# Kernel tuning notes

Hardware: AMD Instinct MI355X
Metric: run time of the kernel (lower is better)

## Reference

```python
import jax, jax.numpy as jnp
import numpy as np

MARGIN = 0.2
EPS = 1e-6  # torch.pairwise_distance default eps added to (x1 - x2)


def setup_inputs() -> dict:
    key = jax.random.key(0)
    k1, k2 = jax.random.split(key)
    N, D = 8192, 128
    x = jax.random.normal(k1, (N, D), dtype=jnp.float32)
    target = jax.random.randint(k2, (N,), 0, 1000)
    return {"x": x, "target": target}


def _pairwise_dist(x):
    # torch.pairwise_distance(x.unsqueeze(0), x.unsqueeze(1)):
    #   diff[i, j] = x[j] - x[i] + EPS ; dist[i, j] = ||diff[i, j]||_2
    # Expanded quadratic form avoids the [N, N, D] diff tensor:
    #   ||a - b + e||^2 = ||a||^2 + ||b||^2 - 2 a.b + 2e*sum(a - b) + D*e^2
    sq = jnp.sum(x * x, axis=1)          # [N]
    s = jnp.sum(x, axis=1)               # [N]
    dot = x @ x.T                        # [N, N]
    D = x.shape[1]
    d2 = (sq[None, :] + sq[:, None] - 2.0 * dot
          + 2.0 * EPS * (s[None, :] - s[:, None]) + D * EPS * EPS)
    return jnp.sqrt(jnp.maximum(d2, 0.0))


def reference(x, target):
    N = x.shape[0]
    dist = _pairwise_dist(x)                                 # [N, N]
    same = target[None, :] == target[:, None]                # [N, N] bool
    pos_mask = (same & ~jnp.eye(N, dtype=bool)).astype(x.dtype)
    hardest_pos = jnp.max(pos_mask * dist, axis=1, keepdims=True)  # [N, 1]
    neg_mask = (~same).astype(x.dtype)
    max_neg = jnp.max(dist, axis=1, keepdims=True)           # [N, 1]
    anchor_neg = dist + max_neg * (1.0 - neg_mask)           # push positives up
    hardest_neg = jnp.min(anchor_neg, axis=1, keepdims=True) # [N, 1]
    loss = jax.nn.relu(hardest_pos - hardest_neg + MARGIN)
    return jnp.mean(loss)
```

## Files before the change

kernel.cpp:

```cpp
#include <hip/hip_runtime.h>

#define N 8192
#define Dk 128
#define EPSC 1e-6f
#define MARGIN 0.2f

#define BI 64
#define BJ 128
#define JSPLIT 4
#define LDA 136

typedef __attribute__((ext_vector_type(8))) short bf16x8;
typedef __attribute__((ext_vector_type(4))) float f32x4;

__device__ __forceinline__ unsigned short f2bf(float f) {
    unsigned u = __float_as_uint(f);
    u = (u + 0x7FFFu + ((u >> 16) & 1u)) >> 16;
    return (unsigned short)u;
}
__device__ __forceinline__ unsigned enc(float f) {
    unsigned u = __float_as_uint(f);
    return (u & 0x80000000u) ? ~u : (u | 0x80000000u);
}
__device__ __forceinline__ float dec(unsigned u) {
    return __uint_as_float((u & 0x80000000u) ? (u & 0x7FFFFFFFu) : ~u);
}

__global__ void prep_kernel(const float* __restrict__ x,
                            unsigned short* __restrict__ Xb,
                            float* __restrict__ P, float* __restrict__ Q,
                            unsigned* __restrict__ wsHp, unsigned* __restrict__ wsMn) {
    int gtid = blockIdx.x * blockDim.x + threadIdx.x;
    int row = gtid >> 6;
    int lane = gtid & 63;
    const float2 v = *reinterpret_cast<const float2*>(&x[row * Dk + lane * 2]);
    float sq = v.x * v.x + v.y * v.y;
    float s = v.x + v.y;
    ushort2 o;
    o.x = f2bf(v.x);
    o.y = f2bf(v.y);
    *reinterpret_cast<ushort2*>(&Xb[row * Dk + lane * 2]) = o;
#pragma unroll
    for (int m = 32; m >= 1; m >>= 1) {
        sq += __shfl_xor(sq, m);
        s += __shfl_xor(s, m);
    }
    if (lane == 0) {
        P[row] = sq - 2.0f * EPSC * s;
        Q[row] = sq + 2.0f * EPSC * s + (float)Dk * EPSC * EPSC;
        wsHp[row] = 0x007FFFFFu;
        wsMn[row] = 0xFF800000u;
    }
}

__global__ __launch_bounds__(256) void main_kernel(
        const unsigned short* __restrict__ Xb,
        const float* __restrict__ Q,
        const int* __restrict__ tgt,
        unsigned* __restrict__ wsHp, unsigned* __restrict__ wsMn) {
    __shared__ unsigned short As[BI * LDA];
    __shared__ unsigned short Bs[BJ * LDA];
    __shared__ float Qs[BJ];
    __shared__ int Ts[BJ];

    const int tid = threadIdx.x;
    const int w = tid >> 6;
    const int lane = tid & 63;
    const int n = lane & 15;
    const int q = lane >> 4;

    const int ig = (int)blockIdx.x >> 2;
    const int js = (int)blockIdx.x & 3;
    const int i0 = ig * BI;
    const int jstart = js * (N / JSPLIT);

    const uint4* Xb4 = reinterpret_cast<const uint4*>(Xb);

#pragma unroll
    for (int it = 0; it < 4; ++it) {
        int idx = tid + 256 * it;
        int r = idx >> 4, c = idx & 15;
        uint4 v = Xb4[(i0 + r) * 16 + c];
        *reinterpret_cast<uint4*>(&As[r * LDA + c * 8]) = v;
    }

    int tslot[16];
#pragma unroll
    for (int ti = 0; ti < 4; ++ti) {
        int4 t4 = *reinterpret_cast<const int4*>(&tgt[i0 + 16 * ti + 4 * q]);
        tslot[ti * 4 + 0] = t4.x;
        tslot[ti * 4 + 1] = t4.y;
        tslot[ti * 4 + 2] = t4.z;
        tslot[ti * 4 + 3] = t4.w;
    }

    float hp[16], mn[16];
#pragma unroll
    for (int s = 0; s < 16; ++s) {
        hp[s] = -INFINITY;
        mn[s] = INFINITY;
    }

    int aoff[4], boff[2];
#pragma unroll
    for (int ti = 0; ti < 4; ++ti) aoff[ti] = (16 * ti + n) * LDA + q * 8;
#pragma unroll
    for (int tj = 0; tj < 2; ++tj) boff[tj] = (32 * w + 16 * tj + n) * LDA + q * 8;

    for (int step = 0; step < (N / JSPLIT) / BJ; ++step) {
        const int jbase = jstart + step * BJ;
        __syncthreads();
#pragma unroll
        for (int it = 0; it < 8; ++it) {
            int idx = tid + 256 * it;
            int r = idx >> 4, c = idx & 15;
            uint4 v = Xb4[(jbase + r) * 16 + c];
            *reinterpret_cast<uint4*>(&Bs[r * LDA + c * 8]) = v;
        }
        if (tid < BJ) Qs[tid] = Q[jbase + tid];
        else Ts[tid - BJ] = tgt[jbase + tid - BJ];
        __syncthreads();

        f32x4 acc[4][2];
#pragma unroll
        for (int ti = 0; ti < 4; ++ti)
#pragma unroll
            for (int tj = 0; tj < 2; ++tj) acc[ti][tj] = 0.0f;

#pragma unroll
        for (int kk = 0; kk < 4; ++kk) {
            bf16x8 b0 = *reinterpret_cast<const bf16x8*>(&Bs[boff[0] + kk * 32]);
            bf16x8 b1 = *reinterpret_cast<const bf16x8*>(&Bs[boff[1] + kk * 32]);
#pragma unroll
            for (int ti = 0; ti < 4; ++ti) {
                bf16x8 a = *reinterpret_cast<const bf16x8*>(&As[aoff[ti] + kk * 32]);
                acc[ti][0] = __builtin_amdgcn_mfma_f32_16x16x32_bf16(a, b0, acc[ti][0], 0, 0, 0);
                acc[ti][1] = __builtin_amdgcn_mfma_f32_16x16x32_bf16(a, b1, acc[ti][1], 0, 0, 0);
            }
        }

#pragma unroll
        for (int tj = 0; tj < 2; ++tj) {
            int col = 32 * w + 16 * tj + n;
            float Qv = Qs[col];
            int tv = Ts[col];
#pragma unroll
            for (int ti = 0; ti < 4; ++ti) {
#pragma unroll
                for (int r = 0; r < 4; ++r) {
                    float val = fmaf(-2.0f, acc[ti][tj][r], Qv);
                    int sidx = ti * 4 + r;
                    bool sm = (tv == tslot[sidx]);
                    hp[sidx] = sm ? fmaxf(hp[sidx], val) : hp[sidx];
                    mn[sidx] = sm ? mn[sidx] : fminf(mn[sidx], val);
                }
            }
        }
    }

#pragma unroll
    for (int m = 1; m <= 8; m <<= 1) {
#pragma unroll
        for (int s = 0; s < 16; ++s) {
            hp[s] = fmaxf(hp[s], __shfl_xor(hp[s], m));
            mn[s] = fminf(mn[s], __shfl_xor(mn[s], m));
        }
    }
    if (n == 0) {
#pragma unroll
        for (int ti = 0; ti < 4; ++ti) {
#pragma unroll
            for (int r = 0; r < 4; ++r) {
                int i = i0 + 16 * ti + 4 * q + r;
                atomicMax(&wsHp[i], enc(hp[ti * 4 + r]));
                atomicMin(&wsMn[i], enc(mn[ti * 4 + r]));
            }
        }
    }
}

__global__ void finish_kernel(const float* __restrict__ P,
                              const unsigned* __restrict__ wsHp,
                              const unsigned* __restrict__ wsMn,
                              float* __restrict__ out) {
    int i = blockIdx.x * 256 + threadIdx.x;
    float Pi = P[i];
    float hp = sqrtf(fmaxf(Pi + dec(wsHp[i]), 0.0f));
    float hn = sqrtf(fmaxf(Pi + dec(wsMn[i]), 0.0f));
    float loss = fmaxf(hp - hn + MARGIN, 0.0f) * (1.0f / (float)N);
#pragma unroll
    for (int m = 32; m >= 1; m >>= 1) loss += __shfl_xor(loss, m);
    __shared__ float wsum[4];
    int lane = threadIdx.x & 63, wv = threadIdx.x >> 6;
    if (lane == 0) wsum[wv] = loss;
    __syncthreads();
    if (threadIdx.x == 0) atomicAdd(out, wsum[0] + wsum[1] + wsum[2] + wsum[3]);
}

extern "C" void kernel_launch(void* const* d_in, const int* in_sizes, int n_in,
                              void* d_out, int out_size, void* d_ws, size_t ws_size,
                              hipStream_t stream) {
    const float* x = (const float*)d_in[0];
    const int* tgt = (const int*)d_in[1];
    float* out = (float*)d_out;

    char* ws = (char*)d_ws;
    const size_t xb_bytes = (size_t)N * Dk * 2;
    unsigned short* Xb = (unsigned short*)ws;
    float* P = (float*)(ws + xb_bytes);
    float* Q = (float*)(ws + xb_bytes + (size_t)N * 4);
    unsigned* wsHp = (unsigned*)(ws + xb_bytes + (size_t)N * 8);
    unsigned* wsMn = (unsigned*)(ws + xb_bytes + (size_t)N * 12);

    hipMemsetAsync(d_out, 0, sizeof(float), stream);
    prep_kernel<<<N / 4, 256, 0, stream>>>(x, Xb, P, Q, wsHp, wsMn);
    main_kernel<<<(N / BI) * JSPLIT, 256, 0, stream>>>(Xb, Q, tgt, wsHp, wsMn);
    finish_kernel<<<N / 256, 256, 0, stream>>>(P, wsHp, wsMn, out);
}
```

Baseline: 103.6 us.

## Rework pairwise-distance kernel with register A tiles, swizzled direct-to-LDS loads, and fused epilogue

The main kernel now uses 128x128 tiles with A fragments held in registers and B tiles loaded straight into LDS through global_load_lds, using an XOR-swizzled layout that the prep kernel writes. The prep kernel also stores a pre-scaled -2x copy, so the accumulator can start at Q and the epilogue needs no FMA, and it packs Q with the target label. The epilogue uses a wave ballot to skip the positive path when no lane shares a label. The finish kernel becomes a single block, which removes the memset and the atomic. The larger register tile raises register pressure, and the extra scaled copy doubles the bf16 workspace.

Result: faster. 98.32 us (-5.1%).

```diff
diff --git a/kernel.cpp b/kernel.cpp
--- a/kernel.cpp
+++ b/kernel.cpp
@@ -5,11 +5,6 @@
 #define EPSC 1e-6f
 #define MARGIN 0.2f
 
-#define BI 64
-#define BJ 128
-#define JSPLIT 4
-#define LDA 136
-
 typedef __attribute__((ext_vector_type(8))) short bf16x8;
 typedef __attribute__((ext_vector_type(4))) float f32x4;
 
@@ -26,72 +21,84 @@
     return __uint_as_float((u & 0x80000000u) ? (u & 0x7FFFFFFFu) : ~u);
 }
 
-__global__ void prep_kernel(const float* __restrict__ x,
-                            unsigned short* __restrict__ Xb,
-                            float* __restrict__ P, float* __restrict__ Q,
+__device__ __forceinline__ void gl_lds16(const void* src, void* lds_dst) {
+    __builtin_amdgcn_global_load_lds(
+        (const __attribute__((address_space(1))) unsigned*)src,
+        (__attribute__((address_space(3))) unsigned*)lds_dst, 16, 0, 0);
+}
+
+__global__ void prep_kernel(const float* __restrict__ x, const int* __restrict__ tgt,
+                            unsigned short* __restrict__ XbA, unsigned short* __restrict__ XbB,
+                            uint2* __restrict__ QT, float* __restrict__ P,
                             unsigned* __restrict__ wsHp, unsigned* __restrict__ wsMn) {
-    int gtid = blockIdx.x * blockDim.x + threadIdx.x;
-    int row = gtid >> 6;
-    int lane = gtid & 63;
-    const float2 v = *reinterpret_cast<const float2*>(&x[row * Dk + lane * 2]);
-    float sq = v.x * v.x + v.y * v.y;
+    int row = blockIdx.x * 4 + (threadIdx.x >> 6);
+    int l = threadIdx.x & 63;
+    const float2 v = *reinterpret_cast<const float2*>(&x[row * Dk + l * 2]);
+    float sq = fmaf(v.x, v.x, v.y * v.y);
     float s = v.x + v.y;
-    ushort2 o;
-    o.x = f2bf(v.x);
-    o.y = f2bf(v.y);
-    *reinterpret_cast<ushort2*>(&Xb[row * Dk + lane * 2]) = o;
+    ushort2 a, b;
+    a.x = f2bf(v.x);
+    a.y = f2bf(v.y);
+    b.x = f2bf(-2.0f * v.x);
+    b.y = f2bf(-2.0f * v.y);
+    int c_phys = (l >> 2) ^ (row & 7);
+    int off = row * Dk + c_phys * 8 + 2 * (l & 3);
+    *reinterpret_cast<ushort2*>(&XbA[off]) = a;
+    *reinterpret_cast<ushort2*>(&XbB[off]) = b;
 #pragma unroll
     for (int m = 32; m >= 1; m >>= 1) {
         sq += __shfl_xor(sq, m);
         s += __shfl_xor(s, m);
     }
-    if (lane == 0) {
+    if (l == 0) {
         P[row] = sq - 2.0f * EPSC * s;
-        Q[row] = sq + 2.0f * EPSC * s + (float)Dk * EPSC * EPSC;
+        uint2 qt;
+        qt.x = __float_as_uint(sq + 2.0f * EPSC * s + (float)Dk * EPSC * EPSC);
+        qt.y = (unsigned)tgt[row];
+        QT[row] = qt;
         wsHp[row] = 0x007FFFFFu;
         wsMn[row] = 0xFF800000u;
     }
 }
 
-__global__ __launch_bounds__(256) void main_kernel(
-        const unsigned short* __restrict__ Xb,
-        const float* __restrict__ Q,
-        const int* __restrict__ tgt,
+__global__ __launch_bounds__(256, 2) void main_kernel(
+        const unsigned short* __restrict__ XbA, const unsigned short* __restrict__ XbB,
+        const uint2* __restrict__ QT, const int* __restrict__ tgt,
         unsigned* __restrict__ wsHp, unsigned* __restrict__ wsMn) {
-    __shared__ unsigned short As[BI * LDA];
-    __shared__ unsigned short Bs[BJ * LDA];
-    __shared__ float Qs[BJ];
-    __shared__ int Ts[BJ];
+    __shared__ unsigned short Bs[128 * Dk];
+    __shared__ uint2 QTs[128];
 
     const int tid = threadIdx.x;
     const int w = tid >> 6;
     const int lane = tid & 63;
     const int n = lane & 15;
     const int q = lane >> 4;
-
-    const int ig = (int)blockIdx.x >> 2;
-    const int js = (int)blockIdx.x & 3;
-    const int i0 = ig * BI;
-    const int jstart = js * (N / JSPLIT);
-
-    const uint4* Xb4 = reinterpret_cast<const uint4*>(Xb);
-
-#pragma unroll
-    for (int it = 0; it < 4; ++it) {
-        int idx = tid + 256 * it;
-        int r = idx >> 4, c = idx & 15;
-        uint4 v = Xb4[(i0 + r) * 16 + c];
-        *reinterpret_cast<uint4*>(&As[r * LDA + c * 8]) = v;
-    }
-
-    int tslot[16];
+    const int wi = w >> 1;
+    const int wj = w & 1;
+    const int sw = n & 7;
+
+    const int ig = (int)blockIdx.x >> 3;
+    const int js = (int)blockIdx.x & 7;
+    const int i0 = ig * 128;
+    const int rbase = i0 + 64 * wi;
+
+    bf16x8 Af[4][4];
 #pragma unroll
     for (int ti = 0; ti < 4; ++ti) {
-        int4 t4 = *reinterpret_cast<const int4*>(&tgt[i0 + 16 * ti + 4 * q]);
-        tslot[ti * 4 + 0] = t4.x;
-        tslot[ti * 4 + 1] = t4.y;
-        tslot[ti * 4 + 2] = t4.z;
-        tslot[ti * 4 + 3] = t4.w;
+        const unsigned short* rp = &XbA[(rbase + 16 * ti + n) * Dk];
+#pragma unroll
+        for (int kk = 0; kk < 4; ++kk)
+            Af[ti][kk] = *reinterpret_cast<const bf16x8*>(&rp[((q + 4 * kk) ^ sw) << 3]);
+    }
+
+    int tsl[16];
+#pragma unroll
+    for (int ti = 0; ti < 4; ++ti) {
+        int4 t4 = *reinterpret_cast<const int4*>(&tgt[rbase + 16 * ti + 4 * q]);
+        tsl[4 * ti + 0] = t4.x;
+        tsl[4 * ti + 1] = t4.y;
+        tsl[4 * ti + 2] = t4.z;
+        tsl[4 * ti + 3] = t4.w;
     }
 
     float hp[16], mn[16];
@@ -101,58 +108,75 @@
         mn[s] = INFINITY;
     }
 
-    int aoff[4], boff[2];
-#pragma unroll
-    for (int ti = 0; ti < 4; ++ti) aoff[ti] = (16 * ti + n) * LDA + q * 8;
-#pragma unroll
-    for (int tj = 0; tj < 2; ++tj) boff[tj] = (32 * w + 16 * tj + n) * LDA + q * 8;
-
-    for (int step = 0; step < (N / JSPLIT) / BJ; ++step) {
-        const int jbase = jstart + step * BJ;
+    for (int step = 0; step < 8; ++step) {
+        const int jbase = js * 1024 + step * 128;
         __syncthreads();
 #pragma unroll
-        for (int it = 0; it < 8; ++it) {
-            int idx = tid + 256 * it;
-            int r = idx >> 4, c = idx & 15;
-            uint4 v = Xb4[(jbase + r) * 16 + c];
-            *reinterpret_cast<uint4*>(&Bs[r * LDA + c * 8]) = v;
-        }
-        if (tid < BJ) Qs[tid] = Q[jbase + tid];
-        else Ts[tid - BJ] = tgt[jbase + tid - BJ];
+        for (int t = 0; t < 8; ++t) {
+            const unsigned short* src = &XbB[(jbase + 32 * w + 4 * t) * Dk] + lane * 8;
+            unsigned short* dst = &Bs[(32 * w + 4 * t) * Dk];
+            gl_lds16(src, dst);
+        }
+        if (w == 0) {
+            const unsigned short* src = reinterpret_cast<const unsigned short*>(&QT[jbase]) + lane * 8;
+            gl_lds16(src, &QTs[0]);
+        }
         __syncthreads();
 
-        f32x4 acc[4][2];
+        float Qv[4];
+        int tv[4];
+#pragma unroll
+        for (int tj = 0; tj < 4; ++tj) {
+            uint2 qt = QTs[64 * wj + 16 * tj + n];
+            Qv[tj] = __uint_as_float(qt.x);
+            tv[tj] = (int)qt.y;
+        }
+
+        f32x4 acc[4][4];
 #pragma unroll
         for (int ti = 0; ti < 4; ++ti)
 #pragma unroll
-            for (int tj = 0; tj < 2; ++tj) acc[ti][tj] = 0.0f;
+            for (int tj = 0; tj < 4; ++tj) acc[ti][tj] = Qv[tj];
 
 #pragma unroll
         for (int kk = 0; kk < 4; ++kk) {
-            bf16x8 b0 = *reinterpret_cast<const bf16x8*>(&Bs[boff[0] + kk * 32]);
-            bf16x8 b1 = *reinterpret_cast<const bf16x8*>(&Bs[boff[1] + kk * 32]);
+            bf16x8 Bf[4];
+#pragma unroll
+            for (int tj = 0; tj < 4; ++tj)
+                Bf[tj] = *reinterpret_cast<const bf16x8*>(
+                    &Bs[(64 * wj + 16 * tj + n) * Dk + (((q + 4 * kk) ^ sw) << 3)]);
+#pragma unroll
+            for (int ti = 0; ti < 4; ++ti)
+#pragma unroll
+                for (int tj = 0; tj < 4; ++tj)
+                    acc[ti][tj] = __builtin_amdgcn_mfma_f32_16x16x32_bf16(Af[ti][kk], Bf[tj],
+                                                                          acc[ti][tj], 0, 0, 0);
+        }
+
+#pragma unroll
+        for (int tj = 0; tj < 4; ++tj) {
+            int tvv = tv[tj];
 #pragma unroll
             for (int ti = 0; ti < 4; ++ti) {
-                bf16x8 a = *reinterpret_cast<const bf16x8*>(&As[aoff[ti] + kk * 32]);
-                acc[ti][0] = __builtin_amdgcn_mfma_f32_16x16x32_bf16(a, b0, acc[ti][0], 0, 0, 0);
-                acc[ti][1] = __builtin_amdgcn_mfma_f32_16x16x32_bf16(a, b1, acc[ti][1], 0, 0, 0);
-            }
-        }
-
-#pragma unroll
-        for (int tj = 0; tj < 2; ++tj) {
-            int col = 32 * w + 16 * tj + n;
-            float Qv = Qs[col];
-            int tv = Ts[col];
-#pragma unroll
-            for (int ti = 0; ti < 4; ++ti) {
-#pragma unroll
-                for (int r = 0; r < 4; ++r) {
-                    float val = fmaf(-2.0f, acc[ti][tj][r], Qv);
-                    int sidx = ti * 4 + r;
-                    bool sm = (tv == tslot[sidx]);
-                    hp[sidx] = sm ? fmaxf(hp[sidx], val) : hp[sidx];
-                    mn[sidx] = sm ? mn[sidx] : fminf(mn[sidx], val);
+                f32x4 v = acc[ti][tj];
+                int e0 = tvv == tsl[4 * ti + 0];
+                int e1 = tvv == tsl[4 * ti + 1];
+                int e2 = tvv == tsl[4 * ti + 2];
+                int e3 = tvv == tsl[4 * ti + 3];
+                if (__ballot(e0 | e1 | e2 | e3)) {
+                    hp[4 * ti + 0] = fmaxf(hp[4 * ti + 0], e0 ? v[0] : -INFINITY);
+                    hp[4 * ti + 1] = fmaxf(hp[4 * ti + 1], e1 ? v[1] : -INFINITY);
+                    hp[4 * ti + 2] = fmaxf(hp[4 * ti + 2], e2 ? v[2] : -INFINITY);
+                    hp[4 * ti + 3] = fmaxf(hp[4 * ti + 3], e3 ? v[3] : -INFINITY);
+                    mn[4 * ti + 0] = fminf(mn[4 * ti + 0], e0 ? INFINITY : v[0]);
+                    mn[4 * ti + 1] = fminf(mn[4 * ti + 1], e1 ? INFINITY : v[1]);
+                    mn[4 * ti + 2] = fminf(mn[4 * ti + 2], e2 ? INFINITY : v[2]);
+                    mn[4 * ti + 3] = fminf(mn[4 * ti + 3], e3 ? INFINITY : v[3]);
+                } else {
+                    mn[4 * ti + 0] = fminf(mn[4 * ti + 0], v[0]);
+                    mn[4 * ti + 1] = fminf(mn[4 * ti + 1], v[1]);
+                    mn[4 * ti + 2] = fminf(mn[4 * ti + 2], v[2]);
+                    mn[4 * ti + 3] = fminf(mn[4 * ti + 3], v[3]);
                 }
             }
         }
@@ -171,9 +195,9 @@
         for (int ti = 0; ti < 4; ++ti) {
 #pragma unroll
             for (int r = 0; r < 4; ++r) {
-                int i = i0 + 16 * ti + 4 * q + r;
-                atomicMax(&wsHp[i], enc(hp[ti * 4 + r]));
-                atomicMin(&wsMn[i], enc(mn[ti * 4 + r]));
+                int i = rbase + 16 * ti + 4 * q + r;
+                atomicMax(&wsHp[i], enc(hp[4 * ti + r]));
+                atomicMin(&wsMn[i], enc(mn[4 * ti + r]));
             }
         }
     }
@@ -183,18 +207,27 @@
                               const unsigned* __restrict__ wsHp,
                               const unsigned* __restrict__ wsMn,
                               float* __restrict__ out) {
-    int i = blockIdx.x * 256 + threadIdx.x;
-    float Pi = P[i];
-    float hp = sqrtf(fmaxf(Pi + dec(wsHp[i]), 0.0f));
-    float hn = sqrtf(fmaxf(Pi + dec(wsMn[i]), 0.0f));
-    float loss = fmaxf(hp - hn + MARGIN, 0.0f) * (1.0f / (float)N);
-#pragma unroll
-    for (int m = 32; m >= 1; m >>= 1) loss += __shfl_xor(loss, m);
-    __shared__ float wsum[4];
-    int lane = threadIdx.x & 63, wv = threadIdx.x >> 6;
-    if (lane == 0) wsum[wv] = loss;
+    int t = threadIdx.x;
+    float sum = 0.0f;
+#pragma unroll
+    for (int k = 0; k < 8; ++k) {
+        int i = t + 1024 * k;
+        float Pi = P[i];
+        float hp = sqrtf(fmaxf(Pi + dec(wsHp[i]), 0.0f));
+        float hn = sqrtf(fmaxf(Pi + dec(wsMn[i]), 0.0f));
+        sum += fmaxf(hp - hn + MARGIN, 0.0f);
+    }
+#pragma unroll
+    for (int m = 32; m >= 1; m >>= 1) sum += __shfl_xor(sum, m);
+    __shared__ float ws[16];
+    if ((t & 63) == 0) ws[t >> 6] = sum;
     __syncthreads();
-    if (threadIdx.x == 0) atomicAdd(out, wsum[0] + wsum[1] + wsum[2] + wsum[3]);
+    if (t == 0) {
+        float tot = 0.0f;
+#pragma unroll
+        for (int i = 0; i < 16; ++i) tot += ws[i];
+        out[0] = tot * (1.0f / (float)N);
+    }
 }
 
 extern "C" void kernel_launch(void* const* d_in, const int* in_sizes, int n_in,
@@ -205,15 +238,15 @@
     float* out = (float*)d_out;
 
     char* ws = (char*)d_ws;
-    const size_t xb_bytes = (size_t)N * Dk * 2;
-    unsigned short* Xb = (unsigned short*)ws;
-    float* P = (float*)(ws + xb_bytes);
-    float* Q = (float*)(ws + xb_bytes + (size_t)N * 4);
-    unsigned* wsHp = (unsigned*)(ws + xb_bytes + (size_t)N * 8);
-    unsigned* wsMn = (unsigned*)(ws + xb_bytes + (size_t)N * 12);
-
-    hipMemsetAsync(d_out, 0, sizeof(float), stream);
-    prep_kernel<<<N / 4, 256, 0, stream>>>(x, Xb, P, Q, wsHp, wsMn);
-    main_kernel<<<(N / BI) * JSPLIT, 256, 0, stream>>>(Xb, Q, tgt, wsHp, wsMn);
-    finish_kernel<<<N / 256, 256, 0, stream>>>(P, wsHp, wsMn, out);
-}
+    const size_t xb = (size_t)N * Dk * 2;
+    unsigned short* XbA = (unsigned short*)ws;
+    unsigned short* XbB = (unsigned short*)(ws + xb);
+    uint2* QT = (uint2*)(ws + 2 * xb);
+    float* P = (float*)(ws + 2 * xb + (size_t)N * 8);
+    unsigned* wsHp = (unsigned*)(ws + 2 * xb + (size_t)N * 12);
+    unsigned* wsMn = (unsigned*)(ws + 2 * xb + (size_t)N * 16);
+
+    prep_kernel<<<N / 4, 256, 0, stream>>>(x, tgt, XbA, XbB, QT, P, wsHp, wsMn);
+    main_kernel<<<512, 256, 0, stream>>>(XbA, XbB, QT, tgt, wsHp, wsMn);
+    finish_kernel<<<1, 1024, 0, stream>>>(P, wsHp, wsMn, out);
+}
```
